# Optimization experiments

Measured on AMD Instinct MI355X. Metric: run time of the kernel, lower is better.

The kernel has to match this reference:

```python
import jax, jax.numpy as jnp
import numpy as np

N = 50000
E = 800000
EP = 200000
IN_C = 128
HID = 128


def setup_inputs() -> dict:
    key = jax.random.key(0)
    ks = jax.random.split(key, 10)
    x = jax.random.normal(ks[0], (N, IN_C), dtype=jnp.float32)
    edge_index = jax.random.randint(ks[1], (2, E), 0, N, dtype=jnp.int64)
    pred_edges = jax.random.randint(ks[2], (2, EP), 0, N, dtype=jnp.int64)
    s_in = 1.0 / np.sqrt(IN_C)
    s_h = 1.0 / np.sqrt(HID)
    W1l = jax.random.normal(ks[3], (IN_C, HID), dtype=jnp.float32) * s_in
    W1r = jax.random.normal(ks[4], (IN_C, HID), dtype=jnp.float32) * s_in
    b1 = jnp.zeros((HID,), dtype=jnp.float32)
    W2l = jax.random.normal(ks[5], (HID, HID), dtype=jnp.float32) * s_h
    W2r = jax.random.normal(ks[6], (HID, HID), dtype=jnp.float32) * s_h
    b2 = jnp.zeros((HID,), dtype=jnp.float32)
    return {"x": x, "W1l": W1l, "b1": b1, "W1r": W1r,
            "W2l": W2l, "b2": b2, "W2r": W2r,
            "edge_index": edge_index, "pred_edges": pred_edges}


def _sage_conv(h, Wl, b, Wr, src, dst, n_nodes):
    # PyG SAGEConv (aggr='mean'): out = lin_l(mean_j x_j) + lin_r(x_i)
    msg = h[src]                                              # (E, D) gather
    agg = jax.ops.segment_sum(msg, dst, num_segments=n_nodes)  # (N, D) scatter-add
    deg = jax.ops.segment_sum(jnp.ones((src.shape[0],), h.dtype), dst,
                              num_segments=n_nodes)
    agg = agg / jnp.maximum(deg, 1.0)[:, None]                # mean (0 for isolated)
    return agg @ Wl + b + h @ Wr


def reference(x, W1l, b1, W1r, W2l, b2, W2r, edge_index, pred_edges):
    n_nodes = x.shape[0]
    src, dst = edge_index[0], edge_index[1]
    h = jax.nn.relu(_sage_conv(x, W1l, b1, W1r, src, dst, n_nodes))
    z = _sage_conv(h, W2l, b2, W2r, src, dst, n_nodes)
    ps, pd = pred_edges[0], pred_edges[1]
    return jnp.sum(z[ps] * z[pd], axis=-1)  # (E_pred,) logits
```

## Files before the change

kernel.cpp:

```cpp
#include <hip/hip_runtime.h>

#define D 128

typedef __attribute__((ext_vector_type(8))) short short8;
typedef __attribute__((ext_vector_type(4))) float f32x4;

__device__ inline unsigned int f2bf_bits(float f) {
    unsigned int u = __float_as_uint(f);
    return (u + 0x7FFFu + ((u >> 16) & 1u)) >> 16;
}

__global__ __launch_bounds__(256) void prep_kernel(
    const float* __restrict__ x,
    const float* __restrict__ W1l, const float* __restrict__ W1r,
    const float* __restrict__ W2l, const float* __restrict__ W2r,
    const int* __restrict__ dst,
    unsigned short* __restrict__ fbf,
    float* __restrict__ xpk,
    unsigned short* __restrict__ w1_hi, unsigned short* __restrict__ w1_lo,
    unsigned short* __restrict__ w2_hi, unsigned short* __restrict__ w2_lo,
    int* __restrict__ part, int* __restrict__ csrpad, int E)
{
    const int t = threadIdx.x;
    const int b = blockIdx.x;
    if (b < 6250) {
        const int i = b * 256 + t;
        const int hw = i >> 5, l5 = i & 31;
        f32x4 v = *(const f32x4*)(x + (size_t)hw * D + l5 * 4);
        ushort4 hv;
        hv.x = (unsigned short)f2bf_bits(v.x);
        hv.y = (unsigned short)f2bf_bits(v.y);
        hv.z = (unsigned short)f2bf_bits(v.z);
        hv.w = (unsigned short)f2bf_bits(v.w);
        *(ushort4*)(fbf + (size_t)hw * D + l5 * 4) = hv;
        const int tile = hw >> 4, r16 = hw & 15;
        const int ks = l5 >> 3, q = (l5 & 7) >> 1, jb = (l5 & 1) * 4;
        const size_t p = ((size_t)(tile * 4 + ks) * 64 + q * 16 + r16) * 8 + jb;
        *(f32x4*)(xpk + p) = v;
    } else if (b < 6506) {
        int gidx = (b - 6250) * 256 + t;
        int sel = gidx >> 15;
        int idx = gidx & 32767;
        int tt = idx >> 12;
        int ks = (idx >> 9) & 7;
        int lane = (idx >> 3) & 63;
        int j = idx & 7;
        int q = lane >> 4, r16 = lane & 15;
        int k = ks * 32 + q * 8 + j;
        int c = tt * 16 + r16;
        const float* Wl = sel ? W2l : W1l;
        const float* Wr = sel ? W2r : W1r;
        float v = (k < 128) ? Wl[k * 128 + c] : Wr[(k - 128) * 128 + c];
        unsigned int h = f2bf_bits(v);
        float hf = __uint_as_float(h << 16);
        unsigned int l = f2bf_bits(v - hf);
        (sel ? w2_hi : w1_hi)[idx] = (unsigned short)h;
        (sel ? w2_lo : w1_lo)[idx] = (unsigned short)l;
    } else if (b < 6570) {
        __shared__ int h[256];
        h[t] = 0;
        __syncthreads();
        const int b3 = b - 6506;
        for (int e = b3 * 256 + t; e < E; e += 64 * 256)
            atomicAdd(&h[dst[e] >> 8], 1);
        __syncthreads();
        part[b3 * 256 + t] = h[t];
    } else {
        if (t < 16) csrpad[t] = 0;
    }
}

__global__ __launch_bounds__(256) void scan256_kernel(const int* __restrict__ part,
                                                      int* __restrict__ cbase,
                                                      int* __restrict__ gcur) {
    __shared__ int wsum[4];
    const int t = threadIdx.x, lane = t & 63, wv = t >> 6;
    int v = 0;
    for (int b = 0; b < 64; ++b) v += part[b * 256 + t];
    int s = v;
#pragma unroll
    for (int o = 1; o < 64; o <<= 1) {
        int u = __shfl_up(s, o, 64);
        if (lane >= o) s += u;
    }
    if (lane == 63) wsum[wv] = s;
    __syncthreads();
    int add = 0;
    for (int w = 0; w < wv; ++w) add += wsum[w];
    cbase[t + 1] = s + add;
    if (t == 0) cbase[0] = 0;
    gcur[t] = s + add - v;
}

#define CCHUNK 4096
__global__ __launch_bounds__(256) void coarse_scatter_kernel(
    const int* __restrict__ src, const int* __restrict__ dst,
    int* __restrict__ gcur, unsigned int* __restrict__ centries, int E)
{
    __shared__ int h[256];
    __shared__ int base[256];
    __shared__ unsigned int stage[CCHUNK];
    const int t = threadIdx.x;
    const int e0 = blockIdx.x * CCHUNK;
    h[t] = 0;
    __syncthreads();
#pragma unroll
    for (int i = 0; i < 16; ++i) {
        int e = e0 + i * 256 + t;
        unsigned int u = 0xFFFFFFFFu;
        if (e < E) {
            int d = dst[e];
            int s = src[e];
            int b = d >> 8;
            u = ((unsigned)b << 24) | ((unsigned)s << 8) | (unsigned)(d & 255);
            atomicAdd(&h[b], 1);
        }
        stage[i * 256 + t] = u;
    }
    __syncthreads();
    base[t] = atomicAdd(&gcur[t], h[t]);
    __syncthreads();
    h[t] = 0;
    __syncthreads();
#pragma unroll
    for (int i = 0; i < 16; ++i) {
        unsigned int u = stage[i * 256 + t];
        if (u != 0xFFFFFFFFu) {
            int b = u >> 24;
            int r = atomicAdd(&h[b], 1);
            int pos = base[b] + r;
            if (pos < E) centries[pos] = u & 0x00FFFFFFu;
        }
    }
}

#define DCAP 8192
__global__ __launch_bounds__(256) void fine_bucket_kernel(
    const unsigned int* __restrict__ centries,
    const int* __restrict__ cbase,
    int* __restrict__ offo, int* __restrict__ csr, int N, int E)
{
    __shared__ int h[256], ex[256], wsum[4];
    __shared__ int stg[DCAP];
    const int t = threadIdx.x, lane = t & 63, wv = t >> 6;
    const int b = blockIdx.x;
    const int s0 = cbase[b];
    const int cnt = cbase[b + 1] - s0;
    h[t] = 0;
    __syncthreads();
    for (int i = t; i < cnt; i += 256)
        atomicAdd(&h[centries[s0 + i] & 255], 1);
    __syncthreads();
    int v = h[t], s = v;
#pragma unroll
    for (int o = 1; o < 64; o <<= 1) {
        int u = __shfl_up(s, o, 64);
        if (lane >= o) s += u;
    }
    if (lane == 63) wsum[wv] = s;
    __syncthreads();
    int add = 0;
    for (int w = 0; w < wv; ++w) add += wsum[w];
    const int exc = s + add - v;
    ex[t] = exc;
    const int dg = b * 256 + t;
    if (dg < N) offo[dg] = s0 + exc;
    if (b == 0 && t == 0) offo[N] = E;
    h[t] = 0;
    __syncthreads();
    if (cnt <= DCAP) {
        for (int i = t; i < cnt; i += 256) {
            unsigned int u = centries[s0 + i];
            int dl = u & 255;
            int r = atomicAdd(&h[dl], 1);
            stg[ex[dl] + r] = (int)(u >> 8);
        }
        __syncthreads();
        for (int i = t; i < cnt; i += 256)
            csr[s0 + i] = stg[i];
    } else {
        for (int i = t; i < cnt; i += 256) {
            unsigned int u = centries[s0 + i];
            int dl = u & 255;
            int r = atomicAdd(&h[dl], 1);
            csr[s0 + ex[dl] + r] = (int)(u >> 8);
        }
    }
}

__global__ __launch_bounds__(256) void gather_mean_kernel(
    const unsigned short* __restrict__ featbf,
    const int* __restrict__ off,
    const int* __restrict__ csr,
    float* __restrict__ aggp)
{
    const int hw = (blockIdx.x * 256 + threadIdx.x) >> 5;
    const int l5 = threadIdx.x & 31;
    const unsigned short* fb = featbf + (size_t)l5 * 4;
    const int start = off[hw];
    const int end = off[hw + 1];
    f32x4 acc = {0.f, 0.f, 0.f, 0.f};
    for (int e = start; e < end; e += 16) {
        int4 ia = *(const int4*)(csr + e);
        int4 ib = *(const int4*)(csr + e + 4);
        int4 ic = *(const int4*)(csr + e + 8);
        int4 id = *(const int4*)(csr + e + 12);
        int sx[16];
        sx[0] = ia.x;  sx[1] = ia.y;  sx[2] = ia.z;  sx[3] = ia.w;
        sx[4] = ib.x;  sx[5] = ib.y;  sx[6] = ib.z;  sx[7] = ib.w;
        sx[8] = ic.x;  sx[9] = ic.y;  sx[10] = ic.z; sx[11] = ic.w;
        sx[12] = id.x; sx[13] = id.y; sx[14] = id.z; sx[15] = id.w;
#pragma unroll
        for (int p = 1; p < 16; ++p) sx[p] = (e + p < end) ? sx[p] : ia.x;
        uint2 r[16];
#pragma unroll
        for (int p = 0; p < 16; ++p) r[p] = *(const uint2*)(fb + (size_t)sx[p] * D);
#pragma unroll
        for (int p = 0; p < 16; ++p) {
            uint2 rv = r[p];
            if (e + p >= end) { rv.x = 0u; rv.y = 0u; }
            acc.x += __uint_as_float(rv.x << 16);
            acc.y += __uint_as_float(rv.x & 0xffff0000u);
            acc.z += __uint_as_float(rv.y << 16);
            acc.w += __uint_as_float(rv.y & 0xffff0000u);
        }
    }
    float dinv = 1.0f / (float)max(end - start, 1);
    acc *= dinv;
    const int tile = hw >> 4, r16 = hw & 15;
    const int ks = l5 >> 3, q = (l5 & 7) >> 1, jb = (l5 & 1) * 4;
    const size_t p = ((size_t)(tile * 4 + ks) * 64 + q * 16 + r16) * 8 + jb;
    *(f32x4*)(aggp + p) = acc;
}

__global__ __launch_bounds__(256) void sage_gemm_kernel(
    const float* __restrict__ aggp,
    const float* __restrict__ selfp,
    const unsigned short* __restrict__ w_hi,
    const unsigned short* __restrict__ w_lo,
    const float* __restrict__ bias,
    float* __restrict__ opk,
    unsigned short* __restrict__ outbf,
    int ntiles, int do_relu)
{
    const int wv = threadIdx.x >> 6;
    const int lane = threadIdx.x & 63;
    const int tile = blockIdx.x * 2 + (wv >> 1);
    const int th = (wv & 1) * 4;
    if (tile >= ntiles) return;
    const int q = lane >> 4, r16 = lane & 15;
    const int n0w = tile * 16;

    f32x4 acc4[4];
#pragma unroll
    for (int t = 0; t < 4; ++t) acc4[t] = (f32x4){0.f, 0.f, 0.f, 0.f};

    const float* ap = aggp + (size_t)tile * 2048 + lane * 8;
    const float* sp = selfp + (size_t)tile * 2048 + lane * 8;

    for (int ks = 0; ks < 8; ++ks) {
        f32x4 a0, a1;
        if (ks < 4) {
            a0 = *(const f32x4*)(ap + ks * 512);
            a1 = *(const f32x4*)(ap + ks * 512 + 4);
        } else {
            a0 = *(const f32x4*)(sp + (ks - 4) * 512);
            a1 = *(const f32x4*)(sp + (ks - 4) * 512 + 4);
        }
        short8 BH[4], BL[4];
        const unsigned short* bh = w_hi + (size_t)(th * 8 + ks) * 512 + lane * 8;
        const unsigned short* bl = w_lo + (size_t)(th * 8 + ks) * 512 + lane * 8;
#pragma unroll
        for (int t = 0; t < 4; ++t) {
            BH[t] = *(const short8*)(bh + (size_t)t * 4096);
            BL[t] = *(const short8*)(bl + (size_t)t * 4096);
        }
        short8 ahi, alo;
#pragma unroll
        for (int i = 0; i < 8; ++i) {
            float vv = (i < 4) ? a0[i] : a1[i - 4];
            unsigned int h = f2bf_bits(vv);
            float hf = __uint_as_float(h << 16);
            unsigned int l = f2bf_bits(vv - hf);
            ahi[i] = (short)h;
            alo[i] = (short)l;
        }
#pragma unroll
        for (int t = 0; t < 4; ++t) {
            acc4[t] = __builtin_amdgcn_mfma_f32_16x16x32_bf16(ahi, BH[t], acc4[t], 0, 0, 0);
            acc4[t] = __builtin_amdgcn_mfma_f32_16x16x32_bf16(alo, BH[t], acc4[t], 0, 0, 0);
            acc4[t] = __builtin_amdgcn_mfma_f32_16x16x32_bf16(ahi, BL[t], acc4[t], 0, 0, 0);
        }
    }

#pragma unroll
    for (int tt = 0; tt < 4; ++tt) {
        const int t = th + tt;
        const float bv = bias[t * 16 + r16];
#pragma unroll
        for (int r = 0; r < 4; ++r) {
            float vv = acc4[tt][r] + bv;
            if (do_relu) vv = fmaxf(vv, 0.f);
            if (opk) {
                const size_t p = ((size_t)(tile * 4 + (t >> 1)) * 64
                                  + ((t & 1) * 2 + (r16 >> 3)) * 16 + q * 4 + r) * 8
                                 + (r16 & 7);
                opk[p] = vv;
            }
            if (outbf) {
                outbf[(size_t)(n0w + q * 4 + r) * D + t * 16 + r16] =
                    (unsigned short)f2bf_bits(vv);
            }
        }
    }
}

__global__ __launch_bounds__(256) void pred_kernel(const unsigned short* __restrict__ zbf,
                                                   const int* __restrict__ ps,
                                                   const int* __restrict__ pd,
                                                   float* __restrict__ out, int EP) {
    int idx = blockIdx.x * blockDim.x + threadIdx.x;
    int e = idx >> 5;
    if (e >= EP) return;
    int l = idx & 31;
    const unsigned short* fb = zbf + (size_t)l * 4;
    uint2 ra = *(const uint2*)(fb + (size_t)ps[e] * D);
    uint2 rb = *(const uint2*)(fb + (size_t)pd[e] * D);
    float p = __uint_as_float(ra.x << 16)         * __uint_as_float(rb.x << 16)
            + __uint_as_float(ra.x & 0xffff0000u) * __uint_as_float(rb.x & 0xffff0000u)
            + __uint_as_float(ra.y << 16)         * __uint_as_float(rb.y << 16)
            + __uint_as_float(ra.y & 0xffff0000u) * __uint_as_float(rb.y & 0xffff0000u);
#pragma unroll
    for (int off = 16; off > 0; off >>= 1) p += __shfl_xor(p, off, 32);
    if (l == 0) out[e] = p;
}

extern "C" void kernel_launch(void* const* d_in, const int* in_sizes, int n_in,
                              void* d_out, int out_size, void* d_ws, size_t ws_size,
                              hipStream_t stream) {
    const float* x   = (const float*)d_in[0];
    const float* W1l = (const float*)d_in[1];
    const float* b1  = (const float*)d_in[2];
    const float* W1r = (const float*)d_in[3];
    const float* W2l = (const float*)d_in[4];
    const float* b2  = (const float*)d_in[5];
    const float* W2r = (const float*)d_in[6];
    const int* edge_index = (const int*)d_in[7];
    const int* pred_edges = (const int*)d_in[8];
    float* out = (float*)d_out;

    const int N  = in_sizes[0] / D;
    const int E  = in_sizes[7] / 2;
    const int EP = in_sizes[8] / 2;

    const int* src = edge_index;
    const int* dst = edge_index + E;
    const int* ps  = pred_edges;
    const int* pd  = pred_edges + EP;

    int* part    = (int*)d_ws;
    int* cbase   = part + 16384;
    int* gcur    = cbase + 272;
    int* off     = gcur + 256;
    unsigned int* centries = (unsigned int*)(off + 50016);
    int* csr     = (int*)(centries + E);
    float* aggp  = (float*)(csr + E + 16);
    float* xpk   = aggp + (size_t)N * D;
    float* hpk   = xpk + (size_t)N * D;
    unsigned short* fbf   = (unsigned short*)(hpk + (size_t)N * D);
    unsigned short* w1_hi = fbf + (size_t)N * D;
    unsigned short* w1_lo = w1_hi + 32768;
    unsigned short* w2_hi = w1_lo + 32768;
    unsigned short* w2_lo = w2_hi + 32768;

    const int nblk_gather = N * 32 / 256;
    const int ntiles = N / 16;
    const int nblk_gemm = (ntiles + 1) / 2;
    const int nbC = (E + CCHUNK - 1) / CCHUNK;
    const int nbD = (N + 255) / 256;

    prep_kernel<<<6571, 256, 0, stream>>>(x, W1l, W1r, W2l, W2r, dst,
                                          fbf, xpk,
                                          w1_hi, w1_lo, w2_hi, w2_lo,
                                          part, csr + E, E);
    scan256_kernel<<<1, 256, 0, stream>>>(part, cbase, gcur);
    coarse_scatter_kernel<<<nbC, 256, 0, stream>>>(src, dst, gcur, centries, E);
    fine_bucket_kernel<<<nbD, 256, 0, stream>>>(centries, cbase, off, csr, N, E);

    gather_mean_kernel<<<nblk_gather, 256, 0, stream>>>(fbf, off, csr, aggp);
    sage_gemm_kernel<<<nblk_gemm, 256, 0, stream>>>(aggp, xpk, w1_hi, w1_lo, b1,
                                                    hpk, fbf, ntiles, 1);
    gather_mean_kernel<<<nblk_gather, 256, 0, stream>>>(fbf, off, csr, aggp);
    sage_gemm_kernel<<<nblk_gemm, 256, 0, stream>>>(aggp, hpk, w2_hi, w2_lo, b2,
                                                    (float*)nullptr, fbf, ntiles, 0);
    pred_kernel<<<(EP * 32 + 255) / 256, 256, 0, stream>>>(fbf, ps, pd, out, EP);
}
```

Before: 265.0 us.

## Store CSR as 16-bit indices with per-node padding to a zero sentinel row

The CSR neighbour list is rebuilt as 16-bit source indices. Each node's segment is padded to a multiple of 16, with pad entries pointing at an extra all-zero feature row (index N), so the gather loop needs no bounds masking. Degrees are stored separately as 16-bit values. This halves index bandwidth and drops per-element compare and select work in the gather. It relies on node ids fitting in 16 bits, which does not hold for N=50000 (ids above 65535 are not possible here, but ids 50000 and up are fine), and it adds per-block slack space and padding writes.

```diff
diff --git a/kernel.cpp b/kernel.cpp
--- a/kernel.cpp
+++ b/kernel.cpp
@@ -19,7 +19,7 @@
     float* __restrict__ xpk,
     unsigned short* __restrict__ w1_hi, unsigned short* __restrict__ w1_lo,
     unsigned short* __restrict__ w2_hi, unsigned short* __restrict__ w2_lo,
-    int* __restrict__ part, int* __restrict__ csrpad, int E)
+    int* __restrict__ part, int N, int E)
 {
     const int t = threadIdx.x;
     const int b = blockIdx.x;
@@ -66,7 +66,7 @@
         __syncthreads();
         part[b3 * 256 + t] = h[t];
     } else {
-        if (t < 16) csrpad[t] = 0;
+        if (t < 64) ((int*)(fbf + (size_t)N * D))[t] = 0;
     }
 }
 
@@ -135,23 +135,29 @@
 }
 
 #define DCAP 8192
+#define SLACK 3856
 __global__ __launch_bounds__(256) void fine_bucket_kernel(
     const unsigned int* __restrict__ centries,
     const int* __restrict__ cbase,
-    int* __restrict__ offo, int* __restrict__ csr, int N, int E)
+    int* __restrict__ offo, unsigned short* __restrict__ deg16,
+    unsigned short* __restrict__ csr16, int N, int E)
 {
     __shared__ int h[256], ex[256], wsum[4];
-    __shared__ int stg[DCAP];
+    __shared__ int tot_sh;
+    __shared__ __align__(16) unsigned short stg[DCAP];
     const int t = threadIdx.x, lane = t & 63, wv = t >> 6;
     const int b = blockIdx.x;
     const int s0 = cbase[b];
     const int cnt = cbase[b + 1] - s0;
+    const int base = ((s0 + 15) & ~15) + b * SLACK;
     h[t] = 0;
     __syncthreads();
     for (int i = t; i < cnt; i += 256)
         atomicAdd(&h[centries[s0 + i] & 255], 1);
     __syncthreads();
-    int v = h[t], s = v;
+    const int v = h[t];
+    const int pdv = (v + 15) & ~15;
+    int s = pdv;
 #pragma unroll
     for (int o = 1; o < 64; o <<= 1) {
         int u = __shfl_up(s, o, 64);
@@ -161,71 +167,78 @@
     __syncthreads();
     int add = 0;
     for (int w = 0; w < wv; ++w) add += wsum[w];
-    const int exc = s + add - v;
+    const int exc = s + add - pdv;
     ex[t] = exc;
+    if (t == 255) tot_sh = exc + pdv;
     const int dg = b * 256 + t;
-    if (dg < N) offo[dg] = s0 + exc;
-    if (b == 0 && t == 0) offo[N] = E;
+    if (dg < N) {
+        offo[dg] = base + exc;
+        deg16[dg] = (unsigned short)v;
+    }
     h[t] = 0;
     __syncthreads();
-    if (cnt <= DCAP) {
+    const int tot = tot_sh;
+    if (tot <= DCAP) {
         for (int i = t; i < cnt; i += 256) {
             unsigned int u = centries[s0 + i];
             int dl = u & 255;
             int r = atomicAdd(&h[dl], 1);
-            stg[ex[dl] + r] = (int)(u >> 8);
+            stg[ex[dl] + r] = (unsigned short)(u >> 8);
         }
         __syncthreads();
-        for (int i = t; i < cnt; i += 256)
-            csr[s0 + i] = stg[i];
+        for (int i = v; i < pdv; ++i) stg[exc + i] = (unsigned short)N;
+        __syncthreads();
+        for (int i = t * 8; i < tot; i += 2048)
+            *(int4*)(csr16 + base + i) = *(const int4*)(stg + i);
     } else {
         for (int i = t; i < cnt; i += 256) {
             unsigned int u = centries[s0 + i];
             int dl = u & 255;
             int r = atomicAdd(&h[dl], 1);
-            csr[s0 + ex[dl] + r] = (int)(u >> 8);
-        }
+            csr16[base + ex[dl] + r] = (unsigned short)(u >> 8);
+        }
+        for (int i = v; i < pdv; ++i) csr16[base + exc + i] = (unsigned short)N;
     }
 }
 
 __global__ __launch_bounds__(256) void gather_mean_kernel(
     const unsigned short* __restrict__ featbf,
     const int* __restrict__ off,
-    const int* __restrict__ csr,
+    const unsigned short* __restrict__ deg16,
+    const unsigned short* __restrict__ csr16,
     float* __restrict__ aggp)
 {
     const int hw = (blockIdx.x * 256 + threadIdx.x) >> 5;
     const int l5 = threadIdx.x & 31;
     const unsigned short* fb = featbf + (size_t)l5 * 4;
     const int start = off[hw];
-    const int end = off[hw + 1];
+    const int dg = deg16[hw];
+    const int pend = start + ((dg + 15) & ~15);
     f32x4 acc = {0.f, 0.f, 0.f, 0.f};
-    for (int e = start; e < end; e += 16) {
-        int4 ia = *(const int4*)(csr + e);
-        int4 ib = *(const int4*)(csr + e + 4);
-        int4 ic = *(const int4*)(csr + e + 8);
-        int4 id = *(const int4*)(csr + e + 12);
+    for (int e = start; e < pend; e += 16) {
+        const int4 w0 = *(const int4*)(csr16 + e);
+        const int4 w1 = *(const int4*)(csr16 + e + 8);
         int sx[16];
-        sx[0] = ia.x;  sx[1] = ia.y;  sx[2] = ia.z;  sx[3] = ia.w;
-        sx[4] = ib.x;  sx[5] = ib.y;  sx[6] = ib.z;  sx[7] = ib.w;
-        sx[8] = ic.x;  sx[9] = ic.y;  sx[10] = ic.z; sx[11] = ic.w;
-        sx[12] = id.x; sx[13] = id.y; sx[14] = id.z; sx[15] = id.w;
-#pragma unroll
-        for (int p = 1; p < 16; ++p) sx[p] = (e + p < end) ? sx[p] : ia.x;
+        sx[0]  = w0.x & 0xffff;  sx[1]  = (unsigned)w0.x >> 16;
+        sx[2]  = w0.y & 0xffff;  sx[3]  = (unsigned)w0.y >> 16;
+        sx[4]  = w0.z & 0xffff;  sx[5]  = (unsigned)w0.z >> 16;
+        sx[6]  = w0.w & 0xffff;  sx[7]  = (unsigned)w0.w >> 16;
+        sx[8]  = w1.x & 0xffff;  sx[9]  = (unsigned)w1.x >> 16;
+        sx[10] = w1.y & 0xffff;  sx[11] = (unsigned)w1.y >> 16;
+        sx[12] = w1.z & 0xffff;  sx[13] = (unsigned)w1.z >> 16;
+        sx[14] = w1.w & 0xffff;  sx[15] = (unsigned)w1.w >> 16;
         uint2 r[16];
 #pragma unroll
         for (int p = 0; p < 16; ++p) r[p] = *(const uint2*)(fb + (size_t)sx[p] * D);
 #pragma unroll
         for (int p = 0; p < 16; ++p) {
-            uint2 rv = r[p];
-            if (e + p >= end) { rv.x = 0u; rv.y = 0u; }
-            acc.x += __uint_as_float(rv.x << 16);
-            acc.y += __uint_as_float(rv.x & 0xffff0000u);
-            acc.z += __uint_as_float(rv.y << 16);
-            acc.w += __uint_as_float(rv.y & 0xffff0000u);
-        }
-    }
-    float dinv = 1.0f / (float)max(end - start, 1);
+            acc.x += __uint_as_float(r[p].x << 16);
+            acc.y += __uint_as_float(r[p].x & 0xffff0000u);
+            acc.z += __uint_as_float(r[p].y << 16);
+            acc.w += __uint_as_float(r[p].y & 0xffff0000u);
+        }
+    }
+    float dinv = 1.0f / (float)max(dg, 1);
     acc *= dinv;
     const int tile = hw >> 4, r16 = hw & 15;
     const int ks = l5 >> 3, q = (l5 & 7) >> 1, jb = (l5 & 1) * 4;
@@ -363,12 +376,13 @@
     int* gcur    = cbase + 272;
     int* off     = gcur + 256;
     unsigned int* centries = (unsigned int*)(off + 50016);
-    int* csr     = (int*)(centries + E);
-    float* aggp  = (float*)(csr + E + 16);
+    unsigned short* csr16  = (unsigned short*)(centries + E);
+    unsigned short* deg16  = csr16 + 1600000;
+    float* aggp  = (float*)(deg16 + 50032);
     float* xpk   = aggp + (size_t)N * D;
     float* hpk   = xpk + (size_t)N * D;
     unsigned short* fbf   = (unsigned short*)(hpk + (size_t)N * D);
-    unsigned short* w1_hi = fbf + (size_t)N * D;
+    unsigned short* w1_hi = fbf + (size_t)(N + 1) * D;
     unsigned short* w1_lo = w1_hi + 32768;
     unsigned short* w2_hi = w1_lo + 32768;
     unsigned short* w2_lo = w2_hi + 32768;
@@ -382,15 +396,15 @@
     prep_kernel<<<6571, 256, 0, stream>>>(x, W1l, W1r, W2l, W2r, dst,
                                           fbf, xpk,
                                           w1_hi, w1_lo, w2_hi, w2_lo,
-                                          part, csr + E, E);
+                                          part, N, E);
     scan256_kernel<<<1, 256, 0, stream>>>(part, cbase, gcur);
     coarse_scatter_kernel<<<nbC, 256, 0, stream>>>(src, dst, gcur, centries, E);
-    fine_bucket_kernel<<<nbD, 256, 0, stream>>>(centries, cbase, off, csr, N, E);
-
-    gather_mean_kernel<<<nblk_gather, 256, 0, stream>>>(fbf, off, csr, aggp);
+    fine_bucket_kernel<<<nbD, 256, 0, stream>>>(centries, cbase, off, deg16, csr16, N, E);
+
+    gather_mean_kernel<<<nblk_gather, 256, 0, stream>>>(fbf, off, deg16, csr16, aggp);
     sage_gemm_kernel<<<nblk_gemm, 256, 0, stream>>>(aggp, xpk, w1_hi, w1_lo, b1,
                                                     hpk, fbf, ntiles, 1);
-    gather_mean_kernel<<<nblk_gather, 256, 0, stream>>>(fbf, off, csr, aggp);
+    gather_mean_kernel<<<nblk_gather, 256, 0, stream>>>(fbf, off, deg16, csr16, aggp);
     sage_gemm_kernel<<<nblk_gemm, 256, 0, stream>>>(aggp, hpk, w2_hi, w2_lo, b2,
                                                     (float*)nullptr, fbf, ntiles, 0);
     pred_kernel<<<(EP * 32 + 255) / 256, 256, 0, stream>>>(fbf, ps, pd, out, EP);
```

After: 282.9 us. +6.8%, slower.
